# Performance work log

Measured on AMD Instinct MI355X. Metric: run time of the kernel, lower is better.

The kernel has to match this reference:

```python
import jax, jax.numpy as jnp
import numpy as np

CAPACITY_RATIO = 0.75  # matches init kwarg


def setup_inputs() -> dict:
    key = jax.random.key(0)
    k1, k2, k3 = jax.random.split(key, 3)
    B, L, D = 4, 8192, 1024
    x = jax.random.normal(k1, (B, L, D), dtype=jnp.float32)
    # router: nn.Linear(dim, 1, bias=False) -> weight vector [D]
    w_router = jax.random.normal(k2, (D,), dtype=jnp.float32) * 0.02
    # block_fn instantiated as GELU(Linear(D, D)) applied to selected tokens
    w_block = jax.random.normal(k3, (D, D), dtype=jnp.float32) * 0.02
    return {"x": x, "w_router": w_router, "w_block": w_block}


def reference(x, w_router, w_block):
    # Inference path of MoDRouter.forward (self.training == False)
    B, L, D = x.shape
    k = max(1, int(L * CAPACITY_RATIO))  # 6144 < L, so routing path taken
    # scores = self.router(x).squeeze(-1)  -> [B, L]
    scores = jnp.einsum('bld,d->bl', x, w_router)
    # top-k token selection per batch row
    _, top_idx = jax.lax.top_k(scores, k)  # [B, k]
    # gather selected tokens: [B, k, D]
    selected = jnp.take_along_axis(x, top_idx[:, :, None], axis=1)
    # block_fn(selected, None): GELU(selected @ w_block)
    processed = jax.nn.gelu(jnp.einsum('bkd,de->bke', selected, w_block))
    # scatter processed tokens back; unselected tokens pass through (residual skip)
    batch_idx = jnp.arange(B)[:, None]  # [B, 1]
    out = x.at[batch_idx, top_idx].set(processed)
    return out
```

## Files before the change

kernel.cpp:

```cpp
#include <hip/hip_runtime.h>
#include <hip/hip_bf16.h>

typedef unsigned short u16;
typedef unsigned int u32;
typedef __attribute__((ext_vector_type(8))) short short8;
typedef __attribute__((ext_vector_type(4))) float f32x4;

#define L_TOK 8192
#define BATCH 4
#define DIM 1024
#define KSEL 6144
#define NTOK (BATCH * L_TOK)
#define NSEL (BATCH * KSEL)
#define NUNSEL (NTOK - NSEL)

__device__ __forceinline__ u16 f2bf(float f) {
    u32 u = __float_as_uint(f);
    return (u16)((u + 0x7fffu + ((u >> 16) & 1u)) >> 16);
}
__device__ __forceinline__ u32 cvt2(float a, float b) {
    __hip_bfloat162 h = __float22bfloat162_rn(float2{a, b});
    u32 r;
    __builtin_memcpy(&r, &h, 4);
    return r;
}
__device__ __forceinline__ float gelu_fast(float v) {
    float z2 = 1.5957691216057308f * (v + 0.044715f * v * v * v);
    return v / (1.0f + __expf(-z2));
}
__device__ __forceinline__ void async_copy16(const void* g, void* l) {
    __builtin_amdgcn_global_load_lds(
        (const __attribute__((address_space(1))) void*)g,
        (__attribute__((address_space(3))) void*)l, 16, 0, 0);
}

__global__ __launch_bounds__(256) void score_kernel(const float* __restrict__ x,
                                                    const float* __restrict__ wr,
                                                    float* __restrict__ scores,
                                                    u16* __restrict__ xb) {
    int token = blockIdx.x * 4 + (threadIdx.x >> 6);
    int lane = threadIdx.x & 63;
    const float4* xr = (const float4*)(x + (size_t)token * DIM) + lane * 4;
    const float4* wp = (const float4*)wr + lane * 4;
    float4 v[4];
    double acc = 0.0;
#pragma unroll
    for (int c = 0; c < 4; ++c) {
        v[c] = xr[c];
        float4 wv = wp[c];
        acc += (double)v[c].x * wv.x + (double)v[c].y * wv.y +
               (double)v[c].z * wv.z + (double)v[c].w * wv.w;
    }
    if (xb) {
        union { short8 s[2]; u32 u[8]; } pk;
        pk.u[0] = cvt2(v[0].x, v[0].y); pk.u[1] = cvt2(v[0].z, v[0].w);
        pk.u[2] = cvt2(v[1].x, v[1].y); pk.u[3] = cvt2(v[1].z, v[1].w);
        pk.u[4] = cvt2(v[2].x, v[2].y); pk.u[5] = cvt2(v[2].z, v[2].w);
        pk.u[6] = cvt2(v[3].x, v[3].y); pk.u[7] = cvt2(v[3].z, v[3].w);
        short8* dst = (short8*)(xb + (size_t)token * DIM + lane * 16);
        dst[0] = pk.s[0]; dst[1] = pk.s[1];
    }
#pragma unroll
    for (int off = 32; off > 0; off >>= 1) acc += __shfl_down(acc, off, 64);
    if (lane == 0) scores[token] = (float)acc;
}

__global__ __launch_bounds__(1024) void select_kernel(const float* __restrict__ scores,
                                                      int* __restrict__ mask,
                                                      int* __restrict__ sel_idx,
                                                      int* __restrict__ unsel_idx) {
    __shared__ u32 keys[L_TOK];
    __shared__ int hist[256];
    __shared__ int g0[256], g1[256];
    __shared__ int wsum[16];
    __shared__ int wsum2[16];
    __shared__ int sel_digit, greater_cnt;
    const int b = blockIdx.x;
    const int tid = threadIdx.x;
    const int lane = tid & 63, wid = tid >> 6;
    const float* s = scores + (size_t)b * L_TOK;
    for (int i = tid; i < L_TOK; i += 1024) {
        u32 u = __float_as_uint(s[i]);
        keys[i] = (u & 0x80000000u) ? ~u : (u | 0x80000000u);
    }

    u32 prefix = 0;
    int need = KSEL;
#pragma unroll
    for (int pass = 0; pass < 4; ++pass) {
        const int shift = 24 - 8 * pass;
        const u32 pmask = (pass == 0) ? 0u : (0xFFFFFFFFu << (shift + 8));
        if (tid < 256) hist[tid] = 0;
        __syncthreads();
        for (int i = tid; i < L_TOK; i += 1024) {
            u32 key = keys[i];
            if ((key & pmask) == prefix)
                atomicAdd(&hist[(key >> shift) & 0xffu], 1);
        }
        __syncthreads();
        if (tid < 256) g0[tid] = hist[tid];
        __syncthreads();
        int* src = g0;
        int* dst = g1;
        for (int step = 1; step < 256; step <<= 1) {
            if (tid < 256) {
                int v = src[tid];
                if (tid + step < 256) v += src[tid + step];
                dst[tid] = v;
            }
            __syncthreads();
            int* t = src; src = dst; dst = t;
        }
        if (tid < 256) {
            int Gd = src[tid];
            int Gn = (tid == 255) ? 0 : src[tid + 1];
            if (Gd >= need && Gn < need) { sel_digit = tid; greater_cnt = Gn; }
        }
        __syncthreads();
        prefix |= ((u32)sel_digit) << shift;
        need -= greater_cnt;
        __syncthreads();
    }
    const u32 T = prefix;
    const int need_eq = need;

    const int base = tid * 8;
    u32 kv[8];
    int eq = 0;
#pragma unroll
    for (int c = 0; c < 8; ++c) { kv[c] = keys[base + c]; eq += (kv[c] == T); }
    int inc = eq;
#pragma unroll
    for (int off = 1; off < 64; off <<= 1) {
        int n = __shfl_up(inc, off, 64);
        if (lane >= off) inc += n;
    }
    if (lane == 63) wsum[wid] = inc;
    __syncthreads();
    int wbase = 0;
    for (int w = 0; w < wid; ++w) wbase += wsum[w];
    int rank = wbase + inc - eq;
    int sel[8];
#pragma unroll
    for (int c = 0; c < 8; ++c) {
        u32 key = kv[c];
        int se = 0;
        if (key > T) se = 1;
        else if (key == T) { se = (rank < need_eq) ? 1 : 0; rank++; }
        sel[c] = se;
    }
    int4* mp = (int4*)(mask + (size_t)b * L_TOK + base);
    mp[0] = int4{sel[0], sel[1], sel[2], sel[3]};
    mp[1] = int4{sel[4], sel[5], sel[6], sel[7]};

    int cnt = 0;
#pragma unroll
    for (int c = 0; c < 8; ++c) cnt += sel[c];
    int inc2 = cnt;
#pragma unroll
    for (int off = 1; off < 64; off <<= 1) {
        int n = __shfl_up(inc2, off, 64);
        if (lane >= off) inc2 += n;
    }
    if (lane == 63) wsum2[wid] = inc2;
    __syncthreads();
    int wb2 = 0;
    for (int w = 0; w < wid; ++w) wb2 += wsum2[w];
    int pos = wb2 + inc2 - cnt;
    int up = base - pos;
    int* si = sel_idx + (size_t)b * KSEL;
    int* ui = unsel_idx + (size_t)b * (L_TOK - KSEL);
#pragma unroll
    for (int c = 0; c < 8; ++c) {
        int gtok = b * L_TOK + base + c;
        if (sel[c]) si[pos++] = gtok;
        else        ui[up++]  = gtok;
    }
}

__global__ __launch_bounds__(256) void transpose_kernel(const float* __restrict__ W,
                                                        u16* __restrict__ WT) {
    __shared__ u16 tile[32][33];
    int bx = blockIdx.x * 32, by = blockIdx.y * 32;
    int tx = threadIdx.x & 31, ty = threadIdx.x >> 5;
    for (int r = ty; r < 32; r += 8)
        tile[r][tx] = f2bf(W[(size_t)(by + r) * DIM + bx + tx]);
    __syncthreads();
    for (int r = ty; r < 32; r += 8)
        WT[(size_t)(bx + r) * DIM + by + tx] = tile[tx][r];
}

#define BM 128
#define BN 128
#define BK 32
#define BK2 64

__global__ __launch_bounds__(256) void gemm_idx_kernel(const u16* __restrict__ Xb,
                                                       const u16* __restrict__ WT,
                                                       const int* __restrict__ sel_idx,
                                                       float* __restrict__ out) {
    __shared__ alignas(16) u16 As[BM * BK2];
    __shared__ alignas(16) u16 Bs[BN * BK2];
    const int tid = threadIdx.x;
    const int wave = tid >> 6, lane = tid & 63;
    const int wm = wave >> 1, wn = wave & 1;
    const int rowbase = blockIdx.x * BM;
    const int colbase = blockIdx.y * BN;
    const int q = lane >> 4, mrow = lane & 15;

    f32x4 acc[4][4] = {};

    const u16* asrc[4];
    const u16* bsrc[4];
    int ldsOff[4];
#pragma unroll
    for (int j = 0; j < 4; ++j) {
        int c = tid + 256 * j;
        int row = c >> 3, slot = c & 7;
        int sslot = slot ^ (row & 7);
        int tok = sel_idx[rowbase + row];
        asrc[j] = Xb + (size_t)tok * DIM + sslot * 8;
        bsrc[j] = WT + (size_t)(colbase + row) * DIM + sslot * 8;
        ldsOff[j] = c * 8;
    }

    for (int kt = 0; kt < DIM; kt += BK2) {
#pragma unroll
        for (int j = 0; j < 4; ++j) async_copy16(asrc[j] + kt, As + ldsOff[j]);
#pragma unroll
        for (int j = 0; j < 4; ++j) async_copy16(bsrc[j] + kt, Bs + ldsOff[j]);
        __syncthreads();

#pragma unroll
        for (int kk = 0; kk < 2; ++kk) {
            short8 a[4], b[4];
#pragma unroll
            for (int i = 0; i < 4; ++i) {
                int r = wm * 64 + i * 16 + mrow;
                int slot = (kk * 4 + q) ^ (r & 7);
                a[i] = *(const short8*)(As + r * BK2 + slot * 8);
            }
#pragma unroll
            for (int j = 0; j < 4; ++j) {
                int r = wn * 64 + j * 16 + mrow;
                int slot = (kk * 4 + q) ^ (r & 7);
                b[j] = *(const short8*)(Bs + r * BK2 + slot * 8);
            }
#pragma unroll
            for (int i = 0; i < 4; ++i)
#pragma unroll
                for (int j = 0; j < 4; ++j)
                    acc[i][j] = __builtin_amdgcn_mfma_f32_16x16x32_bf16(a[i], b[j], acc[i][j], 0, 0, 0);
        }
        __syncthreads();
    }

#pragma unroll
    for (int i = 0; i < 4; ++i) {
#pragma unroll
        for (int r = 0; r < 4; ++r) {
            int lrow = wm * 64 + i * 16 + q * 4 + r;
            int tok = sel_idx[rowbase + lrow];
#pragma unroll
            for (int j = 0; j < 4; ++j) {
                float g = gelu_fast(acc[i][j][r]);
                int col = colbase + wn * 64 + j * 16 + mrow;
                out[(size_t)tok * DIM + col] = g;
            }
        }
    }
}

__global__ __launch_bounds__(256) void gemm_f32_kernel(const float* __restrict__ X,
                                                       const u16* __restrict__ WT,
                                                       const int* __restrict__ mask,
                                                       float* __restrict__ out) {
    __shared__ alignas(16) u16 As[BM * BK];
    __shared__ alignas(16) u16 Bs[BN * BK];
    const int tid = threadIdx.x;
    const int wave = tid >> 6, lane = tid & 63;
    const int wm = wave >> 1, wn = wave & 1;
    const size_t rowbase = (size_t)blockIdx.x * BM;
    const int colbase = blockIdx.y * BN;

    f32x4 acc[4][4] = {};

    const int cb0 = tid, cb1 = tid + 256;
    const int br0 = cb0 >> 2, bk0 = (cb0 & 3) * 8;
    const int br1 = cb1 >> 2, bk1 = (cb1 & 3) * 8;
    const int arow = tid >> 1, ahalf = tid & 1;
    const int q = lane >> 4, mrow = lane & 15;

    for (int kt = 0; kt < DIM; kt += BK) {
        async_copy16(WT + (size_t)(colbase + br0) * DIM + kt + bk0, Bs + cb0 * 8);
        async_copy16(WT + (size_t)(colbase + br1) * DIM + kt + bk1, Bs + cb1 * 8);

        const float4* xp = (const float4*)(X + (rowbase + arow) * DIM + kt + ahalf * 16);
        float4 v0 = xp[0], v1 = xp[1], v2 = xp[2], v3 = xp[3];
        union { short8 s[2]; u32 u[8]; } pk;
        pk.u[0] = cvt2(v0.x, v0.y); pk.u[1] = cvt2(v0.z, v0.w);
        pk.u[2] = cvt2(v1.x, v1.y); pk.u[3] = cvt2(v1.z, v1.w);
        pk.u[4] = cvt2(v2.x, v2.y); pk.u[5] = cvt2(v2.z, v2.w);
        pk.u[6] = cvt2(v3.x, v3.y); pk.u[7] = cvt2(v3.z, v3.w);
        *(short8*)(As + arow * BK + ahalf * 16)     = pk.s[0];
        *(short8*)(As + arow * BK + ahalf * 16 + 8) = pk.s[1];

        __syncthreads();

        short8 a[4], b[4];
#pragma unroll
        for (int i = 0; i < 4; ++i)
            a[i] = *(const short8*)(As + (wm * 64 + i * 16 + mrow) * BK + q * 8);
#pragma unroll
        for (int j = 0; j < 4; ++j)
            b[j] = *(const short8*)(Bs + (wn * 64 + j * 16 + mrow) * BK + q * 8);
#pragma unroll
        for (int i = 0; i < 4; ++i)
#pragma unroll
            for (int j = 0; j < 4; ++j)
                acc[i][j] = __builtin_amdgcn_mfma_f32_16x16x32_bf16(a[i], b[j], acc[i][j], 0, 0, 0);
        __syncthreads();
    }

#pragma unroll
    for (int i = 0; i < 4; ++i) {
#pragma unroll
        for (int r = 0; r < 4; ++r) {
            size_t grow = rowbase + wm * 64 + i * 16 + q * 4 + r;
            if (mask[grow]) {
#pragma unroll
                for (int j = 0; j < 4; ++j) {
                    float g = gelu_fast(acc[i][j][r]);
                    int col = colbase + wn * 64 + j * 16 + mrow;
                    out[grow * DIM + col] = g;
                }
            }
        }
    }
}

__global__ __launch_bounds__(256) void passthrough_idx_kernel(const float* __restrict__ x,
                                                              const int* __restrict__ unsel_idx,
                                                              float* __restrict__ out) {
    int tok = unsel_idx[blockIdx.x];
    size_t c = (size_t)tok * (DIM / 4) + threadIdx.x;
    ((float4*)out)[c] = ((const float4*)x)[c];
}

extern "C" void kernel_launch(void* const* d_in, const int* in_sizes, int n_in,
                              void* d_out, int out_size, void* d_ws, size_t ws_size,
                              hipStream_t stream) {
    const float* x  = (const float*)d_in[0];
    const float* wr = (const float*)d_in[1];
    const float* wb = (const float*)d_in[2];
    float* out = (float*)d_out;

    char* ws = (char*)d_ws;
    float* scores    = (float*)ws;
    int*   mask      = (int*)(ws + (size_t)NTOK * 4);
    int*   sel_idx   = (int*)(ws + (size_t)NTOK * 8);
    int*   unsel_idx = (int*)(ws + (size_t)NTOK * 8 + (size_t)NSEL * 4);
    char*  after_idx = ws + (size_t)NTOK * 8 + (size_t)NTOK * 4;
    u16*   WT        = (u16*)after_idx;
    u16*   Xb        = (u16*)(after_idx + (size_t)DIM * DIM * 2);

    const size_t need_ws = (size_t)NTOK * 12 + (size_t)DIM * DIM * 2
                         + (size_t)NTOK * DIM * 2;
    const bool big = (ws_size >= need_ws);

    score_kernel<<<NTOK / 4, 256, 0, stream>>>(x, wr, scores, big ? Xb : nullptr);
    select_kernel<<<BATCH, 1024, 0, stream>>>(scores, mask, sel_idx, unsel_idx);
    transpose_kernel<<<dim3(DIM / 32, DIM / 32), 256, 0, stream>>>(wb, WT);
    if (big) {
        gemm_idx_kernel<<<dim3(NSEL / BM, DIM / BN), 256, 0, stream>>>(Xb, WT, sel_idx, out);
    } else {
        gemm_f32_kernel<<<dim3(NTOK / BM, DIM / BN), 256, 0, stream>>>(x, WT, mask, out);
    }
    passthrough_idx_kernel<<<NUNSEL, 256, 0, stream>>>(x, unsel_idx, out);
}
```

Baseline: 327.8 us.

## Double-buffer the gathered GEMM with 256x128 tiles and prefetch two stages ahead

Rewrites the selected-token GEMM to use a 256x128 block tile with BK=32 and two LDS buffers. Loads for tile t+2 are issued while MFMAs on tile t run, with explicit vmcnt waits, barriers and sched_barriers, and raised wave priority during the MFMA section. Each wave now holds an 8x4 accumulator grid, which doubles reuse of the B fragments and halves the block count. The costs are higher register pressure (launch_bounds 256,2) and a hand-tuned waitcnt scheme that can break if the number of outstanding loads does not match what the waits assume.

```diff
diff --git a/kernel.cpp b/kernel.cpp
--- a/kernel.cpp
+++ b/kernel.cpp
@@ -190,80 +190,118 @@
         WT[(size_t)(bx + r) * DIM + by + tx] = tile[tx][r];
 }
 
-#define BM 128
-#define BN 128
-#define BK 32
-#define BK2 64
-
-__global__ __launch_bounds__(256) void gemm_idx_kernel(const u16* __restrict__ Xb,
-                                                       const u16* __restrict__ WT,
-                                                       const int* __restrict__ sel_idx,
-                                                       float* __restrict__ out) {
-    __shared__ alignas(16) u16 As[BM * BK2];
-    __shared__ alignas(16) u16 Bs[BN * BK2];
+#define PM 256
+#define PN 128
+#define PK 32
+#define PNT (DIM / PK)
+#define ASZ (PM * PK)
+#define BSZ (PN * PK)
+
+__global__ __launch_bounds__(256, 2) void gemm_idx_kernel(const u16* __restrict__ Xb,
+                                                          const u16* __restrict__ WT,
+                                                          const int* __restrict__ sel_idx,
+                                                          float* __restrict__ out) {
+    __shared__ alignas(16) u16 As[2][ASZ];
+    __shared__ alignas(16) u16 Bs[2][BSZ];
     const int tid = threadIdx.x;
     const int wave = tid >> 6, lane = tid & 63;
     const int wm = wave >> 1, wn = wave & 1;
-    const int rowbase = blockIdx.x * BM;
-    const int colbase = blockIdx.y * BN;
+    const int rowbase = blockIdx.x * PM;
+    const int colbase = blockIdx.y * PN;
     const int q = lane >> 4, mrow = lane & 15;
 
-    f32x4 acc[4][4] = {};
-
-    const u16* asrc[4];
-    const u16* bsrc[4];
-    int ldsOff[4];
+    f32x4 acc[8][4] = {};
+
+    const u16* aS[4]; int aO[4];
+    const u16* bS[2]; int bO[2];
 #pragma unroll
     for (int j = 0; j < 4; ++j) {
         int c = tid + 256 * j;
-        int row = c >> 3, slot = c & 7;
-        int sslot = slot ^ (row & 7);
+        int row = c >> 2, slot = c & 3;
+        int ss = slot ^ (row & 3);
         int tok = sel_idx[rowbase + row];
-        asrc[j] = Xb + (size_t)tok * DIM + sslot * 8;
-        bsrc[j] = WT + (size_t)(colbase + row) * DIM + sslot * 8;
-        ldsOff[j] = c * 8;
-    }
-
-    for (int kt = 0; kt < DIM; kt += BK2) {
-#pragma unroll
-        for (int j = 0; j < 4; ++j) async_copy16(asrc[j] + kt, As + ldsOff[j]);
-#pragma unroll
-        for (int j = 0; j < 4; ++j) async_copy16(bsrc[j] + kt, Bs + ldsOff[j]);
-        __syncthreads();
-
-#pragma unroll
-        for (int kk = 0; kk < 2; ++kk) {
-            short8 a[4], b[4];
-#pragma unroll
-            for (int i = 0; i < 4; ++i) {
-                int r = wm * 64 + i * 16 + mrow;
-                int slot = (kk * 4 + q) ^ (r & 7);
-                a[i] = *(const short8*)(As + r * BK2 + slot * 8);
-            }
+        aS[j] = Xb + (size_t)tok * DIM + ss * 8;
+        aO[j] = c * 8;
+    }
+#pragma unroll
+    for (int j = 0; j < 2; ++j) {
+        int c = tid + 256 * j;
+        int row = c >> 2, slot = c & 3;
+        int ss = slot ^ (row & 3);
+        bS[j] = WT + (size_t)(colbase + row) * DIM + ss * 8;
+        bO[j] = c * 8;
+    }
+
+#pragma unroll
+    for (int tt = 0; tt < 2; ++tt) {
+        int ko = tt * PK;
+#pragma unroll
+        for (int j = 0; j < 4; ++j) async_copy16(aS[j] + ko, &As[tt][aO[j]]);
+#pragma unroll
+        for (int j = 0; j < 2; ++j) async_copy16(bS[j] + ko, &Bs[tt][bO[j]]);
+    }
+    asm volatile("s_waitcnt vmcnt(6)" ::: "memory");
+    __builtin_amdgcn_sched_barrier(0);
+    __builtin_amdgcn_s_barrier();
+    __builtin_amdgcn_sched_barrier(0);
+
+    const int xorv = (q ^ (mrow & 3)) * 8;
+
+    for (int t = 0; t < PNT; ++t) {
+        const u16* Ac = As[t & 1];
+        const u16* Bc = Bs[t & 1];
+        short8 a[8], b[4];
+#pragma unroll
+        for (int i = 0; i < 8; ++i) {
+            int r = wm * 128 + i * 16 + mrow;
+            a[i] = *(const short8*)(Ac + r * PK + xorv);
+        }
+#pragma unroll
+        for (int j = 0; j < 4; ++j) {
+            int r = wn * 64 + j * 16 + mrow;
+            b[j] = *(const short8*)(Bc + r * PK + xorv);
+        }
+        asm volatile("s_waitcnt lgkmcnt(0)" ::: "memory");
+        __builtin_amdgcn_sched_barrier(0);
+        __builtin_amdgcn_s_barrier();
+        __builtin_amdgcn_sched_barrier(0);
+
+        {
+            int ts = (t + 2 < PNT) ? t + 2 : t;
+            int ko = ts * PK;
+            u16* Aw = As[t & 1];
+            u16* Bw = Bs[t & 1];
+#pragma unroll
+            for (int j = 0; j < 4; ++j) async_copy16(aS[j] + ko, Aw + aO[j]);
+#pragma unroll
+            for (int j = 0; j < 2; ++j) async_copy16(bS[j] + ko, Bw + bO[j]);
+        }
+        __builtin_amdgcn_sched_barrier(0);
+
+        __builtin_amdgcn_s_setprio(1);
+#pragma unroll
+        for (int i = 0; i < 8; ++i)
+#pragma unroll
+            for (int j = 0; j < 4; ++j)
+                acc[i][j] = __builtin_amdgcn_mfma_f32_16x16x32_bf16(a[i], b[j], acc[i][j], 0, 0, 0);
+        __builtin_amdgcn_s_setprio(0);
+        __builtin_amdgcn_sched_barrier(0);
+
+        asm volatile("s_waitcnt vmcnt(6)" ::: "memory");
+        __builtin_amdgcn_sched_barrier(0);
+        __builtin_amdgcn_s_barrier();
+        __builtin_amdgcn_sched_barrier(0);
+    }
+
+#pragma unroll
+    for (int i = 0; i < 8; ++i) {
+#pragma unroll
+        for (int rr = 0; rr < 4; ++rr) {
+            int lrow = wm * 128 + i * 16 + q * 4 + rr;
+            int tok = sel_idx[rowbase + lrow];
 #pragma unroll
             for (int j = 0; j < 4; ++j) {
-                int r = wn * 64 + j * 16 + mrow;
-                int slot = (kk * 4 + q) ^ (r & 7);
-                b[j] = *(const short8*)(Bs + r * BK2 + slot * 8);
-            }
-#pragma unroll
-            for (int i = 0; i < 4; ++i)
-#pragma unroll
-                for (int j = 0; j < 4; ++j)
-                    acc[i][j] = __builtin_amdgcn_mfma_f32_16x16x32_bf16(a[i], b[j], acc[i][j], 0, 0, 0);
-        }
-        __syncthreads();
-    }
-
-#pragma unroll
-    for (int i = 0; i < 4; ++i) {
-#pragma unroll
-        for (int r = 0; r < 4; ++r) {
-            int lrow = wm * 64 + i * 16 + q * 4 + r;
-            int tok = sel_idx[rowbase + lrow];
-#pragma unroll
-            for (int j = 0; j < 4; ++j) {
-                float g = gelu_fast(acc[i][j][r]);
+                float g = gelu_fast(acc[i][j][rr]);
                 int col = colbase + wn * 64 + j * 16 + mrow;
                 out[(size_t)tok * DIM + col] = g;
             }
@@ -271,17 +309,20 @@
     }
 }
 
+#define FBM 128
+#define FBN 128
+#define FBK 32
 __global__ __launch_bounds__(256) void gemm_f32_kernel(const float* __restrict__ X,
                                                        const u16* __restrict__ WT,
                                                        const int* __restrict__ mask,
                                                        float* __restrict__ out) {
-    __shared__ alignas(16) u16 As[BM * BK];
-    __shared__ alignas(16) u16 Bs[BN * BK];
+    __shared__ alignas(16) u16 Asf[FBM * FBK];
+    __shared__ alignas(16) u16 Bsf[FBN * FBK];
     const int tid = threadIdx.x;
     const int wave = tid >> 6, lane = tid & 63;
     const int wm = wave >> 1, wn = wave & 1;
-    const size_t rowbase = (size_t)blockIdx.x * BM;
-    const int colbase = blockIdx.y * BN;
+    const size_t rowbase = (size_t)blockIdx.x * FBM;
+    const int colbase = blockIdx.y * FBN;
 
     f32x4 acc[4][4] = {};
 
@@ -291,9 +332,9 @@
     const int arow = tid >> 1, ahalf = tid & 1;
     const int q = lane >> 4, mrow = lane & 15;
 
-    for (int kt = 0; kt < DIM; kt += BK) {
-        async_copy16(WT + (size_t)(colbase + br0) * DIM + kt + bk0, Bs + cb0 * 8);
-        async_copy16(WT + (size_t)(colbase + br1) * DIM + kt + bk1, Bs + cb1 * 8);
+    for (int kt = 0; kt < DIM; kt += FBK) {
+        async_copy16(WT + (size_t)(colbase + br0) * DIM + kt + bk0, Bsf + cb0 * 8);
+        async_copy16(WT + (size_t)(colbase + br1) * DIM + kt + bk1, Bsf + cb1 * 8);
 
         const float4* xp = (const float4*)(X + (rowbase + arow) * DIM + kt + ahalf * 16);
         float4 v0 = xp[0], v1 = xp[1], v2 = xp[2], v3 = xp[3];
@@ -302,18 +343,18 @@
         pk.u[2] = cvt2(v1.x, v1.y); pk.u[3] = cvt2(v1.z, v1.w);
         pk.u[4] = cvt2(v2.x, v2.y); pk.u[5] = cvt2(v2.z, v2.w);
         pk.u[6] = cvt2(v3.x, v3.y); pk.u[7] = cvt2(v3.z, v3.w);
-        *(short8*)(As + arow * BK + ahalf * 16)     = pk.s[0];
-        *(short8*)(As + arow * BK + ahalf * 16 + 8) = pk.s[1];
+        *(short8*)(Asf + arow * FBK + ahalf * 16)     = pk.s[0];
+        *(short8*)(Asf + arow * FBK + ahalf * 16 + 8) = pk.s[1];
 
         __syncthreads();
 
         short8 a[4], b[4];
 #pragma unroll
         for (int i = 0; i < 4; ++i)
-            a[i] = *(const short8*)(As + (wm * 64 + i * 16 + mrow) * BK + q * 8);
+            a[i] = *(const short8*)(Asf + (wm * 64 + i * 16 + mrow) * FBK + q * 8);
 #pragma unroll
         for (int j = 0; j < 4; ++j)
-            b[j] = *(const short8*)(Bs + (wn * 64 + j * 16 + mrow) * BK + q * 8);
+            b[j] = *(const short8*)(Bsf + (wn * 64 + j * 16 + mrow) * FBK + q * 8);
 #pragma unroll
         for (int i = 0; i < 4; ++i)
 #pragma unroll
@@ -372,9 +413,9 @@
     select_kernel<<<BATCH, 1024, 0, stream>>>(scores, mask, sel_idx, unsel_idx);
     transpose_kernel<<<dim3(DIM / 32, DIM / 32), 256, 0, stream>>>(wb, WT);
     if (big) {
-        gemm_idx_kernel<<<dim3(NSEL / BM, DIM / BN), 256, 0, stream>>>(Xb, WT, sel_idx, out);
+        gemm_idx_kernel<<<dim3(NSEL / PM, DIM / PN), 256, 0, stream>>>(Xb, WT, sel_idx, out);
     } else {
-        gemm_f32_kernel<<<dim3(NTOK / BM, DIM / BN), 256, 0, stream>>>(x, WT, mask, out);
+        gemm_f32_kernel<<<dim3(NTOK / FBM, DIM / FBN), 256, 0, stream>>>(x, WT, mask, out);
     }
     passthrough_idx_kernel<<<NUNSEL, 256, 0, stream>>>(x, unsel_idx, out);
 }
```

Result: no change. 331.5 us (+1.1%).
